# Kernel tuning notes

Hardware: AMD Instinct MI355X
Metric: run time of the kernel (lower is better)

The kernel has to match this reference:

```python
import jax, jax.numpy as jnp
import numpy as np

FIXED_SIZE = (160, 160, 160)

def _reference_grid(grid_size):
    # [d1, d2, d3, 3] float32 grid of voxel indices, as in layer_util.get_reference_grid
    ax = [jnp.arange(d, dtype=jnp.float32) for d in grid_size]
    return jnp.stack(jnp.meshgrid(*ax, indexing="ij"), axis=-1)

def _resample_linear(vol, loc):
    # vol: [B, D1, D2, D3]; loc: [B, f1, f2, f3, 3] (voxel coords in vol space)
    B = vol.shape[0]
    dims = vol.shape[1:4]
    max_f = jnp.asarray([d - 1 for d in dims], dtype=loc.dtype)
    max_i = jnp.asarray([d - 1 for d in dims], dtype=jnp.int32)
    locc = jnp.clip(loc, 0.0, max_f)          # clamp to volume bounds
    lo = jnp.floor(locc)
    w = locc - lo                              # trilinear weights in [0,1]
    i0 = lo.astype(jnp.int32)
    i1 = jnp.minimum(i0 + 1, max_i)
    b = jnp.arange(B).reshape(B, 1, 1, 1)
    x0, y0, z0 = i0[..., 0], i0[..., 1], i0[..., 2]
    x1, y1, z1 = i1[..., 0], i1[..., 1], i1[..., 2]
    wx, wy, wz = w[..., 0], w[..., 1], w[..., 2]
    ux, uy, uz = 1.0 - wx, 1.0 - wy, 1.0 - wz
    g = lambda ix, iy, iz: vol[b, ix, iy, iz]  # 8-neighbor gather
    return (g(x0, y0, z0) * ux * uy * uz +
            g(x0, y0, z1) * ux * uy * wz +
            g(x0, y1, z0) * ux * wy * uz +
            g(x0, y1, z1) * ux * wy * wz +
            g(x1, y0, z0) * wx * uy * uz +
            g(x1, y0, z1) * wx * uy * wz +
            g(x1, y1, z0) * wx * wy * uz +
            g(x1, y1, z1) * wx * wy * wz)

def setup_inputs() -> dict:
    key = jax.random.key(0)
    k1, k2 = jax.random.split(key)
    B = 4
    ddf = jax.random.normal(k1, (B,) + FIXED_SIZE + (3,), dtype=jnp.float32)
    image = jax.random.normal(k2, (B,) + FIXED_SIZE, dtype=jnp.float32)
    return {"ddf": ddf, "image": image}

def reference(ddf, image):
    grid_ref = _reference_grid(FIXED_SIZE)[None]      # [1, f1, f2, f3, 3]
    grid_warped = grid_ref + ddf                      # [B, f1, f2, f3, 3]
    return _resample_linear(image, grid_warped)       # [B, f1, f2, f3]
```

## Files before the change

kernel.cpp:

```cpp
#include <hip/hip_runtime.h>

#define D     160
#define D2    (D * D)
#define D3    (D * D * D)
#define NB    4
#define TL    4
#define ZSL   32
#define ZWIN  40
#define WINX  12
#define RING  28
#define PLANE 480
#define LDSF  (RING * PLANE)
#define TPB   256
#define NWAVE 4
#define TPDX  (D / TL)
#define TPDZ  (D / ZSL)
#define NRUN  4
#define NBLK  (NB * TPDX * TPDZ * NRUN)

typedef float f32x2 __attribute__((ext_vector_type(2)));
typedef int   i32x2 __attribute__((ext_vector_type(2)));

struct AState {
    f32x2 wx2, wy2, wz2;
    int ba[2], bc[2];
    int pk[2];
    unsigned flags;
};

__device__ __forceinline__ void phaseA(
    float xgf, float ygf, float zgf,
    int xwb, int ywb, int zwb, int su,
    f32x2 q0, f32x2 q1, f32x2 q2, AState& S)
{
    const f32x2 zero2 = {0.0f, 0.0f};
    const f32x2 max2  = {(float)(D - 1), (float)(D - 1)};
    f32x2 dx = {q0.x, q1.y};
    f32x2 dy = {q0.y, q2.x};
    f32x2 dz = {q1.x, q2.y};
    f32x2 xg2 = {xgf, xgf};
    f32x2 yg2 = {ygf, ygf};
    f32x2 zg2 = {zgf, zgf + 1.0f};

    f32x2 fx2 = __builtin_elementwise_min(
                    __builtin_elementwise_max(xg2 + dx, zero2), max2);
    f32x2 fy2 = __builtin_elementwise_min(
                    __builtin_elementwise_max(yg2 + dy, zero2), max2);
    f32x2 fz2 = __builtin_elementwise_min(
                    __builtin_elementwise_max(zg2 + dz, zero2), max2);

    i32x2 X0 = __builtin_convertvector(fx2, i32x2);
    i32x2 Y0 = __builtin_convertvector(fy2, i32x2);
    i32x2 Z0 = __builtin_convertvector(fz2, i32x2);
    S.wx2 = fx2 - __builtin_convertvector(X0, f32x2);
    S.wy2 = fy2 - __builtin_convertvector(Y0, f32x2);
    S.wz2 = fz2 - __builtin_convertvector(Z0, f32x2);

    S.flags = 0;
#pragma unroll
    for (int j = 0; j < 2; ++j) {
        int x0 = X0[j], y0 = Y0[j], z0 = Z0[j];
        int sx0 = x0 - xwb, sy0 = y0 - ywb, sz0 = z0 - zwb;
        bool inWin = ((unsigned)sx0 <= 10u) & ((unsigned)sy0 <= 10u) &
                     ((unsigned)sz0 <= 38u);
        S.flags |= (unsigned)inWin << j;
        int csx = min(max(sx0, 0), 10);
        int csy = min(max(sy0, 0), 10);
        int csz = min(max(sz0, 0), 38);
        int t0 = su + csy; if (t0 >= RING) t0 -= RING;
        int t1 = t0 + 1;   if (t1 == RING) t1 = 0;
        S.ba[j] = t0 * PLANE + csx * ZWIN + csz;
        S.bc[j] = t1 * PLANE + csx * ZWIN + csz;
        S.pk[j] = x0 | (y0 << 8) | (z0 << 16);
    }
}

__device__ __forceinline__ f32x2 phaseB(const float* __restrict__ buf,
                                        const float* __restrict__ vol,
                                        const AState& S)
{
    const f32x2 one2 = {1.0f, 1.0f};
    float a0s[2], a1s[2], c0s[2], c1s[2], e0s[2], e1s[2], g0s[2], g1s[2];
#pragma unroll
    for (int j = 0; j < 2; ++j) {
        a0s[j] = buf[S.ba[j]];          a1s[j] = buf[S.ba[j] + 1];
        c0s[j] = buf[S.bc[j]];          c1s[j] = buf[S.bc[j] + 1];
        e0s[j] = buf[S.ba[j] + ZWIN];   e1s[j] = buf[S.ba[j] + ZWIN + 1];
        g0s[j] = buf[S.bc[j] + ZWIN];   g1s[j] = buf[S.bc[j] + ZWIN + 1];
        if (!((S.flags >> j) & 1)) {
            int x0 = S.pk[j] & 255;
            int y0 = (S.pk[j] >> 8) & 255;
            int z0 = S.pk[j] >> 16;
            int x1 = min(x0 + 1, D - 1);
            int y1 = min(y0 + 1, D - 1);
            int zc = min(z0, D - 2);
            bool sh = z0 > zc;
            f32x2 f00 = *(const f32x2*)(vol + x0 * D2 + y0 * D + zc);
            f32x2 f01 = *(const f32x2*)(vol + x0 * D2 + y1 * D + zc);
            f32x2 f10 = *(const f32x2*)(vol + x1 * D2 + y0 * D + zc);
            f32x2 f11 = *(const f32x2*)(vol + x1 * D2 + y1 * D + zc);
            a0s[j] = sh ? f00.y : f00.x;  a1s[j] = f00.y;
            c0s[j] = sh ? f01.y : f01.x;  c1s[j] = f01.y;
            e0s[j] = sh ? f10.y : f10.x;  e1s[j] = f10.y;
            g0s[j] = sh ? f11.y : f11.x;  g1s[j] = f11.y;
        }
    }
    f32x2 A0 = {a0s[0], a0s[1]}, A1 = {a1s[0], a1s[1]};
    f32x2 C0 = {c0s[0], c0s[1]}, C1 = {c1s[0], c1s[1]};
    f32x2 E0 = {e0s[0], e0s[1]}, E1 = {e1s[0], e1s[1]};
    f32x2 G0 = {g0s[0], g0s[1]}, G1 = {g1s[0], g1s[1]};

    f32x2 ux2 = one2 - S.wx2, uy2 = one2 - S.wy2, uz2 = one2 - S.wz2;
    return (A0 * uz2 + A1 * S.wz2) * (ux2 * uy2)
         + (C0 * uz2 + C1 * S.wz2) * (ux2 * S.wy2)
         + (E0 * uz2 + E1 * S.wz2) * (S.wx2 * uy2)
         + (G0 * uz2 + G1 * S.wz2) * (S.wx2 * S.wy2);
}

__global__ __launch_bounds__(TPB) void warp_kernel(
    const float* __restrict__ ddf,
    const float* __restrict__ image,
    float* __restrict__ out)
{
    extern __shared__ float buf[];

    const int tid  = threadIdx.x;
    const int w    = tid >> 6;
    const int lane = tid & 63;
    const int row  = tid >> 4;
    const int zch  = tid & 15;
    const int rx   = row >> 2, ry = row & 3, zbl = zch * 2;

    int g    = blockIdx.x;
    int gx8  = (g & 7) * (NBLK / 8) + (g >> 3);
    int yrun = gx8 & 3;
    int t    = gx8 >> 2;
    int zi   = t % TPDZ;  t /= TPDZ;
    int xi   = t % TPDX;
    int b    = t / TPDX;

    const int yt0    = yrun * 40;
    const int xt     = xi * TL, zl = zi * ZSL;
    const int xwb    = xt - 4,  zwb = zl - 4;
    const int volofs = b * D3;
    const float* vol = image + volofs;

    int pfix[2];
#pragma unroll
    for (int k = 0; k < 2; ++k) {
        int f  = k * 256 + lane * 4;
        int sx = f / ZWIN;
        int zo = f - sx * ZWIN;
        int srcx = min(max(xwb + sx, 0), D - 1);
        int srcz = min(max(zwb + zo, 0), D - 4);
        pfix[k] = volofs + srcx * D2 + srcz;
    }

    int su  = yt0 % RING;
    int ywb = yt0 - 4;

    int   vb  = volofs + (xt + rx) * D2 + (yt0 + ry) * D + (zl + zbl);
    float ygf = (float)(yt0 + ry);
    const float xgf = (float)(xt + rx);
    const float zgf = (float)(zl + zbl);

    const int kk = w & 1;

#pragma unroll
    for (int m = 0; m < 8; ++m) {
        int L  = w + m * NWAVE;
        int pi = L >> 1, k = L & 1;
        int p  = ywb + pi;
        int srcy = max(p, 0);
        int slot = su + pi; if (slot >= RING) slot -= RING;
        if (k == 0 || lane < 56) {
            const float* gp = image + pfix[k] + srcy * D;
            __builtin_amdgcn_global_load_lds(
                (const __attribute__((address_space(1))) void*)gp,
                (__attribute__((address_space(3))) void*)(buf + slot * PLANE + k * 256),
                16, 0, 0);
        }
    }
    f32x2 qa0, qa1, qa2, qb0, qb1, qb2;
    f32x2 na0 = {0,0}, na1 = {0,0}, na2 = {0,0};
    f32x2 nb0 = {0,0}, nb1 = {0,0}, nb2 = {0,0};
    {
        const float* p = ddf + (size_t)vb * 3;
        qa0 = __builtin_nontemporal_load((const f32x2*)p);
        qa1 = __builtin_nontemporal_load((const f32x2*)(p + 2));
        qa2 = __builtin_nontemporal_load((const f32x2*)(p + 4));
        const float* p2 = ddf + (size_t)(vb + TL * D) * 3;
        qb0 = __builtin_nontemporal_load((const f32x2*)p2);
        qb1 = __builtin_nontemporal_load((const f32x2*)(p2 + 2));
        qb2 = __builtin_nontemporal_load((const f32x2*)(p2 + 4));
    }
    asm volatile("s_waitcnt vmcnt(0)" ::: "memory");
    __builtin_amdgcn_sched_barrier(0);
    __builtin_amdgcn_s_barrier();
    __builtin_amdgcn_sched_barrier(0);

#pragma unroll 1
    for (int d = 0; d < 5; ++d) {
        const bool more = (d < 4);

        if (more) {
#pragma unroll
            for (int s = 0; s < 4; ++s) {
                int pi = (w >> 1) + s * 2;
                int p  = ywb + 16 + pi;
                int srcy = min(p, D - 1);
                int slot = su + 16 + pi; if (slot >= RING) slot -= RING;
                if (kk == 0 || lane < 56) {
                    const float* gp = image + pfix[kk] + srcy * D;
                    __builtin_amdgcn_global_load_lds(
                        (const __attribute__((address_space(1))) void*)gp,
                        (__attribute__((address_space(3))) void*)(buf + slot * PLANE + kk * 256),
                        16, 0, 0);
                }
            }
        }
        __builtin_amdgcn_sched_barrier(0);

        int su4 = su + 4; if (su4 >= RING) su4 -= RING;
        AState Sa, Sb;
        phaseA(xgf, ygf,        zgf, xwb, ywb,     zwb, su,  qa0, qa1, qa2, Sa);
        phaseA(xgf, ygf + 4.0f, zgf, xwb, ywb + 4, zwb, su4, qb0, qb1, qb2, Sb);
        __builtin_amdgcn_sched_barrier(0);

        if (more) {
            const float* p = ddf + (size_t)(vb + 8 * D) * 3;
            na0 = __builtin_nontemporal_load((const f32x2*)p);
            na1 = __builtin_nontemporal_load((const f32x2*)(p + 2));
            na2 = __builtin_nontemporal_load((const f32x2*)(p + 4));
            const float* p2 = ddf + (size_t)(vb + 12 * D) * 3;
            nb0 = __builtin_nontemporal_load((const f32x2*)p2);
            nb1 = __builtin_nontemporal_load((const f32x2*)(p2 + 2));
            nb2 = __builtin_nontemporal_load((const f32x2*)(p2 + 4));
        }
        __builtin_amdgcn_sched_barrier(0);

        f32x2 ra = phaseB(buf, vol, Sa);
        f32x2 rb = phaseB(buf, vol, Sb);
        __builtin_nontemporal_store(ra, (f32x2*)(out + vb));
        __builtin_nontemporal_store(rb, (f32x2*)(out + vb + 4 * D));
        __builtin_amdgcn_sched_barrier(0);

        if (more) {
            asm volatile("s_waitcnt vmcnt(8)" ::: "memory");
            __builtin_amdgcn_sched_barrier(0);
            __builtin_amdgcn_s_barrier();
            __builtin_amdgcn_sched_barrier(0);

            qa0 = na0; qa1 = na1; qa2 = na2;
            qb0 = nb0; qb1 = nb1; qb2 = nb2;
            vb += 8 * D; ygf += 8.0f; ywb += 8;
            su += 8; if (su >= RING) su -= RING;
        }
    }
}

extern "C" void kernel_launch(void* const* d_in, const int* in_sizes, int n_in,
                              void* d_out, int out_size, void* d_ws, size_t ws_size,
                              hipStream_t stream) {
    const float* ddf   = (const float*)d_in[0];
    const float* image = (const float*)d_in[1];
    float* out = (float*)d_out;

    warp_kernel<<<NBLK, TPB, LDSF * sizeof(float), stream>>>(ddf, image, out);
}
```

Before: 81.70 us.

## Shrink LDS ring to 20 planes and split per-step prefetch into two halves

Reduces the y-plane ring buffer from 28 to 20 planes, cutting LDS per block, and restructures the per-step prefetch into two halves. One half is issued before phase A and one after the next ddf loads, with an extra wait and barrier before phase B. The smaller LDS footprint is meant to allow more resident blocks per CU. In exchange it adds a second barrier per step and tighter prefetch distance, which may expose more load latency.

Measured after the change: 82.42 us. No clear change (+0.9%).

```diff
diff --git a/kernel.cpp b/kernel.cpp
--- a/kernel.cpp
+++ b/kernel.cpp
@@ -8,7 +8,7 @@
 #define ZSL   32
 #define ZWIN  40
 #define WINX  12
-#define RING  28
+#define RING  20
 #define PLANE 480
 #define LDSF  (RING * PLANE)
 #define TPB   256
@@ -156,7 +156,7 @@
         pfix[k] = volofs + srcx * D2 + srcz;
     }
 
-    int su  = yt0 % RING;
+    int su  = 0;
     int ywb = yt0 - 4;
 
     int   vb  = volofs + (xt + rx) * D2 + (yt0 + ry) * D + (zl + zbl);
@@ -167,12 +167,12 @@
     const int kk = w & 1;
 
 #pragma unroll
-    for (int m = 0; m < 8; ++m) {
+    for (int m = 0; m < 6; ++m) {
         int L  = w + m * NWAVE;
         int pi = L >> 1, k = L & 1;
         int p  = ywb + pi;
         int srcy = max(p, 0);
-        int slot = su + pi; if (slot >= RING) slot -= RING;
+        int slot = pi;
         if (k == 0 || lane < 56) {
             const float* gp = image + pfix[k] + srcy * D;
             __builtin_amdgcn_global_load_lds(
@@ -203,13 +203,14 @@
     for (int d = 0; d < 5; ++d) {
         const bool more = (d < 4);
 
-        if (more) {
-#pragma unroll
-            for (int s = 0; s < 4; ++s) {
+        {
+            int ps = su + 12; if (ps >= RING) ps -= RING;
+#pragma unroll
+            for (int s = 0; s < 2; ++s) {
                 int pi = (w >> 1) + s * 2;
-                int p  = ywb + 16 + pi;
-                int srcy = min(p, D - 1);
-                int slot = su + 16 + pi; if (slot >= RING) slot -= RING;
+                int p  = ywb + 12 + pi;
+                int srcy = min(max(p, 0), D - 1);
+                int slot = ps + pi; if (slot >= RING) slot -= RING;
                 if (kk == 0 || lane < 56) {
                     const float* gp = image + pfix[kk] + srcy * D;
                     __builtin_amdgcn_global_load_lds(
@@ -236,7 +237,29 @@
             nb0 = __builtin_nontemporal_load((const f32x2*)p2);
             nb1 = __builtin_nontemporal_load((const f32x2*)(p2 + 2));
             nb2 = __builtin_nontemporal_load((const f32x2*)(p2 + 4));
-        }
+            __builtin_amdgcn_sched_barrier(0);
+            int ps = su + 16; if (ps >= RING) ps -= RING;
+#pragma unroll
+            for (int s = 0; s < 2; ++s) {
+                int pi = (w >> 1) + s * 2;
+                int p  = ywb + 16 + pi;
+                int srcy = min(max(p, 0), D - 1);
+                int slot = ps + pi; if (slot >= RING) slot -= RING;
+                if (kk == 0 || lane < 56) {
+                    const float* gp = image + pfix[kk] + srcy * D;
+                    __builtin_amdgcn_global_load_lds(
+                        (const __attribute__((address_space(1))) void*)gp,
+                        (__attribute__((address_space(3))) void*)(buf + slot * PLANE + kk * 256),
+                        16, 0, 0);
+                }
+            }
+        }
+        __builtin_amdgcn_sched_barrier(0);
+
+        if (more) { asm volatile("s_waitcnt vmcnt(8)" ::: "memory"); }
+        else      { asm volatile("s_waitcnt vmcnt(0)" ::: "memory"); }
+        __builtin_amdgcn_sched_barrier(0);
+        __builtin_amdgcn_s_barrier();
         __builtin_amdgcn_sched_barrier(0);
 
         f32x2 ra = phaseB(buf, vol, Sa);
@@ -246,7 +269,7 @@
         __builtin_amdgcn_sched_barrier(0);
 
         if (more) {
-            asm volatile("s_waitcnt vmcnt(8)" ::: "memory");
+            asm volatile("s_waitcnt vmcnt(4)" ::: "memory");
             __builtin_amdgcn_sched_barrier(0);
             __builtin_amdgcn_s_barrier();
             __builtin_amdgcn_sched_barrier(0);
```
